# Performance work log

Hardware: AMD Instinct MI355X
Metric: run time of the kernel (lower is better)

The kernel has to match this reference:

```python
import jax, jax.numpy as jnp
import numpy as np

H = 512        # num_hidden
Z = 512        # latent_len
TIME = 0.2
N_STEPS = 4    # fixed-step RK4 replaces adaptive dopri5 (same dynamics math)
B, N = 4, 4096


def _linear_params(k, fin, fout):
    k1, k2 = jax.random.split(k)
    s = 1.0 / np.sqrt(fin)
    W = jax.random.uniform(k1, (fout, fin), minval=-s, maxval=s, dtype=jnp.float32)
    b = jax.random.uniform(k2, (fout,), minval=-s, maxval=s, dtype=jnp.float32)
    return W, b


def setup_inputs() -> dict:
    key = jax.random.key(0)
    ks = jax.random.split(key, 16)
    inp = {
        "code": jax.random.normal(ks[0], (B, 1, Z), dtype=jnp.float32),
        "x": jax.random.uniform(ks[1], (B, N, 3), dtype=jnp.float32),
    }
    dims = {"l1": (3, H), "l2": (H, H), "l3": (H, H), "l4": (H, 3), "cond": (Z, H)}
    i = 2
    for f in ("f1", "f2"):
        for name, (fin, fout) in dims.items():
            W, b = _linear_params(ks[i], fin, fout)
            i += 1
            inp[f + "_" + name + "_w"] = W
            inp[f + "_" + name + "_b"] = b
    return inp


def _node_block(x, sf, W1, b1, W2, b2, W3, b3, W4, b4):
    """Fixed-step RK4 integration of ODEFunc dynamics over [0, TIME].
    x: (B,N,3) point state; sf: (B,1,H) precomputed tanh(cond(code)) shape features
    (constant along the trajectory since the latent code has zero dynamics)."""
    def dyn(p):
        pf = jax.nn.relu(p @ W1.T + b1)          # (B,N,H) point features
        h = pf * sf                               # gated point-shape features
        h = jax.nn.relu(h @ W2.T + b2) + h        # residual stage 1
        h = jax.nn.relu(h @ W3.T + b3) + h        # residual stage 2
        return jnp.tanh(h @ W4.T + b4)            # (B,N,3) flow direction

    dt = TIME / N_STEPS
    def step(p, _):
        k1 = dyn(p)
        k2 = dyn(p + 0.5 * dt * k1)
        k3 = dyn(p + 0.5 * dt * k2)
        k4 = dyn(p + dt * k3)
        return p + (dt / 6.0) * (k1 + 2.0 * k2 + 2.0 * k3 + k4), None

    x, _ = jax.lax.scan(step, x, None, length=N_STEPS)
    return x


def reference(code, x,
              f1_l1_w, f1_l1_b, f1_l2_w, f1_l2_b, f1_l3_w, f1_l3_b,
              f1_l4_w, f1_l4_b, f1_cond_w, f1_cond_b,
              f2_l1_w, f2_l1_b, f2_l2_w, f2_l2_b, f2_l3_w, f2_l3_b,
              f2_l4_w, f2_l4_b, f2_cond_w, f2_cond_b):
    sf1 = jnp.tanh(code @ f1_cond_w.T + f1_cond_b)  # (B,1,H), broadcasts over N
    x = _node_block(x, sf1, f1_l1_w, f1_l1_b, f1_l2_w, f1_l2_b,
                    f1_l3_w, f1_l3_b, f1_l4_w, f1_l4_b)
    sf2 = jnp.tanh(code @ f2_cond_w.T + f2_cond_b)
    x = _node_block(x, sf2, f2_l1_w, f2_l1_b, f2_l2_w, f2_l2_b,
                    f2_l3_w, f2_l3_b, f2_l4_w, f2_l4_b)
    return x  # pred_y: (B,N,3)
```

## Files before the change

### kernel.cpp

```cpp
#include <hip/hip_runtime.h>
#include <stdint.h>

typedef short short8 __attribute__((ext_vector_type(8)));
typedef float floatx16 __attribute__((ext_vector_type(16)));

#define NPTS 16384
#define TILE_M 64
#define THREADS 1024
#define PA 2
#define PB 4

__device__ inline unsigned short f2bf(float f) {
  __bf16 h = (__bf16)f;
  return __builtin_bit_cast(unsigned short, h);
}
__device__ inline float bf2f(unsigned short h) {
  union { unsigned u; float f; } v; v.u = ((unsigned)h) << 16;
  return v.f;
}

__global__
__attribute__((amdgpu_flat_work_group_size(THREADS, THREADS),
               amdgpu_waves_per_eu(4, 4)))
void node_kernel(
    const float* __restrict__ x, float* __restrict__ outp,
    const unsigned short* __restrict__ wbf, const float* __restrict__ sfall,
    const float* __restrict__ w1a, const float* __restrict__ b1a,
    const float* __restrict__ b2a, const float* __restrict__ b3a,
    const float* __restrict__ w4a, const float* __restrict__ b4a,
    const float* __restrict__ w1b, const float* __restrict__ b1b,
    const float* __restrict__ b2b, const float* __restrict__ b3b,
    const float* __restrict__ w4b, const float* __restrict__ b4b)
{
  __shared__ unsigned short act[TILE_M][520];
  __shared__ float pcur4[TILE_M][4];
  __shared__ float pev4[TILE_M][4];
  __shared__ float kac4[TILE_M][4];
  __shared__ float w4s[3][512];

  const int tid = threadIdx.x;
  const int wg = blockIdx.x;
  const int m0 = wg * TILE_M;
  const int batch = wg >> 6;
  const int lane = tid & 63;
  const int wid = tid >> 6;

  if (tid < TILE_M * 3) {
    int m = tid / 3, c = tid % 3;
    float v = x[m0 * 3 + tid];
    pcur4[m][c] = v;
    pev4[m][c] = v;
  }
  __syncthreads();

  const int aBase = (lane & 31) * 1040 + (lane >> 5) * 16;
  const char* actB = (const char*)&act[0][0];
  const int bcol = wid * 64 + lane;

  const int p1col = tid & 511;
  const int p1r0 = (tid >> 9) * 32;

  const float dt = 0.05f;

  #pragma unroll 1
  for (int f = 0; f < 2; ++f) {
    const float* w1 = f ? w1b : w1a;
    const float* b1v = f ? b1b : b1a;
    const float* b2v = f ? b2b : b2a;
    const float* b3v = f ? b3b : b3a;
    const float* w4 = f ? w4b : w4a;
    const float* b4v = f ? b4b : b4a;
    const short8* w2p = (const short8*)(wbf + (size_t)(f * 2 + 0) * 262144) + bcol;
    const short8* w3p = (const short8*)(wbf + (size_t)(f * 2 + 1) * 262144) + bcol;

    const float ww0 = w1[p1col * 3 + 0], ww1 = w1[p1col * 3 + 1], ww2 = w1[p1col * 3 + 2];
    const float bb = b1v[p1col];
    const float ss = sfall[f * 2048 + batch * 512 + p1col];
    const float b40 = b4v[0], b41 = b4v[1], b42 = b4v[2];

    for (int i = tid; i < 1536; i += THREADS) ((float*)w4s)[i] = w4[i];
    __syncthreads();

    #pragma unroll 1
    for (int st = 0; st < 4; ++st) {
      #pragma unroll 1
      for (int stage = 0; stage < 4; ++stage) {
        short8 bq[PB];
        #pragma unroll
        for (int i = 0; i < PB - 1; ++i) bq[i] = w2p[i * 1024];

        #pragma unroll 4
        for (int mi = 0; mi < 32; ++mi) {
          int m = p1r0 + mi;
          const float4 pv = *(const float4*)&pev4[m][0];
          float v = fmaf(pv.x, ww0, fmaf(pv.y, ww1, fmaf(pv.z, ww2, bb)));
          v = fmaxf(v, 0.f) * ss;
          act[m][p1col] = f2bf(v);
        }
        __syncthreads();

        #pragma unroll 1
        for (int s = 0; s < 2; ++s) {
          const float* bias = s ? b3v : b2v;
          const short8* bp = s ? w3p : w2p;
          floatx16 acc0{}, acc1{};
          short8 aq0[PA], aq1[PA];
          #pragma unroll
          for (int i = 0; i < PA - 1; ++i) {
            aq0[i] = *(const short8*)(actB + aBase + i * 32);
            aq1[i] = *(const short8*)(actB + aBase + 33280 + i * 32);
          }

          #pragma unroll
          for (int kt = 0; kt < 32; ++kt) {
            int la = kt + PA - 1;
            if (la < 32) {
              aq0[la % PA] = *(const short8*)(actB + aBase + la * 32);
              aq1[la % PA] = *(const short8*)(actB + aBase + 33280 + la * 32);
            }
            int lb = kt + PB - 1;
            if (lb < 32) bq[lb % PB] = bp[lb * 1024];
            acc0 = __builtin_amdgcn_mfma_f32_32x32x16_bf16(aq0[kt % PA], bq[kt % PB], acc0, 0, 0, 0);
            acc1 = __builtin_amdgcn_mfma_f32_32x32x16_bf16(aq1[kt % PA], bq[kt % PB], acc1, 0, 0, 0);
          }

          if (s == 0) {
            #pragma unroll
            for (int i = 0; i < PB - 1; ++i) bq[i] = w3p[i * 1024];
          }

          __syncthreads();
          {
            int ncol = wid * 32 + (lane & 31);
            float bs = bias[ncol];
            int rbase = 4 * (lane >> 5);
            #pragma unroll
            for (int g = 0; g < 4; ++g) {
              float r0[4], r1[4];
              #pragma unroll
              for (int i = 0; i < 4; ++i) {
                int row = i + 8 * g + rbase;
                r0[i] = bf2f(act[row][ncol]);
                r1[i] = bf2f(act[32 + row][ncol]);
              }
              #pragma unroll
              for (int i = 0; i < 4; ++i) {
                int row = i + 8 * g + rbase;
                float v = fmaxf(acc0[g * 4 + i] + bs, 0.f) + r0[i];
                act[row][ncol] = f2bf(v);
                v = fmaxf(acc1[g * 4 + i] + bs, 0.f) + r1[i];
                act[32 + row][ncol] = f2bf(v);
              }
            }
          }
          __syncthreads();
        }

        {
          int m = tid >> 4, jj = tid & 15;
          const unsigned short* arow = &act[m][0];
          float s0 = 0.f, s1 = 0.f, s2 = 0.f;
          #pragma unroll
          for (int c = 0; c < 4; ++c) {
            int k0 = (c * 16 + jj) * 8;
            short8 av = *(const short8*)(arow + k0);
            #pragma unroll
            for (int half = 0; half < 2; ++half) {
              float4 wv0 = *(const float4*)&w4s[0][k0 + half * 4];
              float4 wv1 = *(const float4*)&w4s[1][k0 + half * 4];
              float4 wv2 = *(const float4*)&w4s[2][k0 + half * 4];
              #pragma unroll
              for (int e = 0; e < 4; ++e) {
                float a = bf2f((unsigned short)av[half * 4 + e]);
                s0 = fmaf(a, ((const float*)&wv0)[e], s0);
                s1 = fmaf(a, ((const float*)&wv1)[e], s1);
                s2 = fmaf(a, ((const float*)&wv2)[e], s2);
              }
            }
          }
          s0 += __shfl_xor(s0, 1); s1 += __shfl_xor(s1, 1); s2 += __shfl_xor(s2, 1);
          s0 += __shfl_xor(s0, 2); s1 += __shfl_xor(s1, 2); s2 += __shfl_xor(s2, 2);
          s0 += __shfl_xor(s0, 4); s1 += __shfl_xor(s1, 4); s2 += __shfl_xor(s2, 4);
          s0 += __shfl_xor(s0, 8); s1 += __shfl_xor(s1, 8); s2 += __shfl_xor(s2, 8);
          if (jj < 3) {
            float sv = (jj == 0) ? s0 : ((jj == 1) ? s1 : s2);
            float bv = (jj == 0) ? b40 : ((jj == 1) ? b41 : b42);
            float fl = tanhf(sv + bv);
            float pc = pcur4[m][jj];
            if (stage == 0) {
              kac4[m][jj] = fl;
              pev4[m][jj] = fmaf(0.5f * dt, fl, pc);
            } else if (stage == 1) {
              kac4[m][jj] += 2.f * fl;
              pev4[m][jj] = fmaf(0.5f * dt, fl, pc);
            } else if (stage == 2) {
              kac4[m][jj] += 2.f * fl;
              pev4[m][jj] = fmaf(dt, fl, pc);
            } else {
              float np = fmaf(dt / 6.f, kac4[m][jj] + fl, pc);
              pcur4[m][jj] = np;
              pev4[m][jj] = np;
            }
          }
        }
        __syncthreads();
      }
    }
  }

  if (tid < TILE_M * 3) outp[m0 * 3 + tid] = pcur4[tid / 3][tid % 3];
}

__global__ void setup_shuffle(const float* s0, const float* s1, const float* s2,
                              const float* s3, unsigned short* dst) {
  int idx = blockIdx.x * blockDim.x + threadIdx.x;
  int w = idx >> 15;
  int r = idx & 32767;
  int lane = r & 63;
  int tile = r >> 6;
  int nt = tile & 15, kt = tile >> 4;
  const float* W = (w == 0) ? s0 : (w == 1) ? s1 : (w == 2) ? s2 : s3;
  int n = nt * 32 + (lane & 31);
  int k0 = kt * 16 + (lane >> 5) * 8;
  const float* src = W + n * 512 + k0;
  unsigned short* d = dst + ((size_t)w << 18) + (size_t)r * 8;
  #pragma unroll
  for (int j = 0; j < 8; ++j) d[j] = f2bf(src[j]);
}

__global__ void setup_sf(const float* code, const float* cw1, const float* cb1,
                         const float* cw2, const float* cb2, float* sfout) {
  int f = blockIdx.x >> 2, b = blockIdx.x & 3;
  const float* cw = f ? cw2 : cw1;
  const float* cb = f ? cb2 : cb1;
  int j = threadIdx.x;
  const float* c = code + b * 512;
  float s = cb[j];
  for (int k = 0; k < 512; ++k) s = fmaf(c[k], cw[j * 512 + k], s);
  sfout[f * 2048 + b * 512 + j] = tanhf(s);
}

extern "C" void kernel_launch(void* const* d_in, const int* in_sizes, int n_in,
                              void* d_out, int out_size, void* d_ws, size_t ws_size,
                              hipStream_t stream) {
  const float* code = (const float*)d_in[0];
  const float* x    = (const float*)d_in[1];
  char* ws = (char*)d_ws;
  float* sf = (float*)ws;
  unsigned short* wbf = (unsigned short*)(ws + 16384);

  setup_shuffle<<<512, 256, 0, stream>>>((const float*)d_in[4], (const float*)d_in[6],
                                         (const float*)d_in[14], (const float*)d_in[16], wbf);
  setup_sf<<<8, 512, 0, stream>>>(code, (const float*)d_in[10], (const float*)d_in[11],
                                  (const float*)d_in[20], (const float*)d_in[21], sf);

  node_kernel<<<NPTS / TILE_M, THREADS, 0, stream>>>(x, (float*)d_out, wbf, sf,
      (const float*)d_in[2], (const float*)d_in[3], (const float*)d_in[5],
      (const float*)d_in[7], (const float*)d_in[8], (const float*)d_in[9],
      (const float*)d_in[12], (const float*)d_in[13], (const float*)d_in[15],
      (const float*)d_in[17], (const float*)d_in[18], (const float*)d_in[19]);
}
```

Baseline: 835.7 us.

## Split MFMA tiles by row-half so each wave reuses A across two column tiles

Each wave previously computed two 32-row tiles against one 32-column weight tile, loading two A fragments and one B fragment per k-step. Now each wave owns one 32-row half and two column tiles, loading one A fragment from LDS and two B fragments from global per k-step. This cuts LDS reads for A but doubles the per-wave global weight fragment loads and the registers held for B prefetch. It also rearranges the W4 copy in shared memory into a padded per-chunk layout, which may change bank conflicts in the final projection.

```diff
diff --git a/kernel.cpp b/kernel.cpp
--- a/kernel.cpp
+++ b/kernel.cpp
@@ -36,7 +36,7 @@
   __shared__ float pcur4[TILE_M][4];
   __shared__ float pev4[TILE_M][4];
   __shared__ float kac4[TILE_M][4];
-  __shared__ float w4s[3][512];
+  __shared__ float w4c[64][28];
 
   const int tid = threadIdx.x;
   const int wg = blockIdx.x;
@@ -44,6 +44,8 @@
   const int batch = wg >> 6;
   const int lane = tid & 63;
   const int wid = tid >> 6;
+  const int rowhalf = wid & 1;
+  const int cp = wid >> 1;
 
   if (tid < TILE_M * 3) {
     int m = tid / 3, c = tid % 3;
@@ -53,9 +55,10 @@
   }
   __syncthreads();
 
-  const int aBase = (lane & 31) * 1040 + (lane >> 5) * 16;
+  const int aBase = (lane & 31) * 1040 + (lane >> 5) * 16 + rowhalf * 33280;
   const char* actB = (const char*)&act[0][0];
-  const int bcol = wid * 64 + lane;
+  const int bcol0 = cp * 128 + lane;
+  const int bcol1 = bcol0 + 64;
 
   const int p1col = tid & 511;
   const int p1r0 = (tid >> 9) * 32;
@@ -70,24 +73,32 @@
     const float* b3v = f ? b3b : b3a;
     const float* w4 = f ? w4b : w4a;
     const float* b4v = f ? b4b : b4a;
-    const short8* w2p = (const short8*)(wbf + (size_t)(f * 2 + 0) * 262144) + bcol;
-    const short8* w3p = (const short8*)(wbf + (size_t)(f * 2 + 1) * 262144) + bcol;
+    const short8* w2p0 = (const short8*)(wbf + (size_t)(f * 2 + 0) * 262144) + bcol0;
+    const short8* w2p1 = (const short8*)(wbf + (size_t)(f * 2 + 0) * 262144) + bcol1;
+    const short8* w3p0 = (const short8*)(wbf + (size_t)(f * 2 + 1) * 262144) + bcol0;
+    const short8* w3p1 = (const short8*)(wbf + (size_t)(f * 2 + 1) * 262144) + bcol1;
 
     const float ww0 = w1[p1col * 3 + 0], ww1 = w1[p1col * 3 + 1], ww2 = w1[p1col * 3 + 2];
     const float bb = b1v[p1col];
     const float ss = sfall[f * 2048 + batch * 512 + p1col];
     const float b40 = b4v[0], b41 = b4v[1], b42 = b4v[2];
 
-    for (int i = tid; i < 1536; i += THREADS) ((float*)w4s)[i] = w4[i];
+    for (int i = tid; i < 64 * 24; i += THREADS) {
+      int q = i / 24, r = i % 24;
+      w4c[q][r] = w4[(r >> 3) * 512 + q * 8 + (r & 7)];
+    }
     __syncthreads();
 
     #pragma unroll 1
     for (int st = 0; st < 4; ++st) {
       #pragma unroll 1
       for (int stage = 0; stage < 4; ++stage) {
-        short8 bq[PB];
+        short8 bq0[PB], bq1[PB];
         #pragma unroll
-        for (int i = 0; i < PB - 1; ++i) bq[i] = w2p[i * 1024];
+        for (int i = 0; i < PB - 1; ++i) {
+          bq0[i] = w2p0[i * 1024];
+          bq1[i] = w2p1[i * 1024];
+        }
 
         #pragma unroll 4
         for (int mi = 0; mi < 32; ++mi) {
@@ -102,54 +113,58 @@
         #pragma unroll 1
         for (int s = 0; s < 2; ++s) {
           const float* bias = s ? b3v : b2v;
-          const short8* bp = s ? w3p : w2p;
+          const short8* bp0 = s ? w3p0 : w2p0;
+          const short8* bp1 = s ? w3p1 : w2p1;
           floatx16 acc0{}, acc1{};
-          short8 aq0[PA], aq1[PA];
+          short8 aq[PA];
           #pragma unroll
-          for (int i = 0; i < PA - 1; ++i) {
-            aq0[i] = *(const short8*)(actB + aBase + i * 32);
-            aq1[i] = *(const short8*)(actB + aBase + 33280 + i * 32);
-          }
+          for (int i = 0; i < PA - 1; ++i)
+            aq[i] = *(const short8*)(actB + aBase + i * 32);
 
           #pragma unroll
           for (int kt = 0; kt < 32; ++kt) {
             int la = kt + PA - 1;
-            if (la < 32) {
-              aq0[la % PA] = *(const short8*)(actB + aBase + la * 32);
-              aq1[la % PA] = *(const short8*)(actB + aBase + 33280 + la * 32);
-            }
+            if (la < 32)
+              aq[la % PA] = *(const short8*)(actB + aBase + la * 32);
             int lb = kt + PB - 1;
-            if (lb < 32) bq[lb % PB] = bp[lb * 1024];
-            acc0 = __builtin_amdgcn_mfma_f32_32x32x16_bf16(aq0[kt % PA], bq[kt % PB], acc0, 0, 0, 0);
-            acc1 = __builtin_amdgcn_mfma_f32_32x32x16_bf16(aq1[kt % PA], bq[kt % PB], acc1, 0, 0, 0);
+            if (lb < 32) {
+              bq0[lb % PB] = bp0[lb * 1024];
+              bq1[lb % PB] = bp1[lb * 1024];
+            }
+            acc0 = __builtin_amdgcn_mfma_f32_32x32x16_bf16(aq[kt % PA], bq0[kt % PB], acc0, 0, 0, 0);
+            acc1 = __builtin_amdgcn_mfma_f32_32x32x16_bf16(aq[kt % PA], bq1[kt % PB], acc1, 0, 0, 0);
           }
 
           if (s == 0) {
             #pragma unroll
-            for (int i = 0; i < PB - 1; ++i) bq[i] = w3p[i * 1024];
+            for (int i = 0; i < PB - 1; ++i) {
+              bq0[i] = w3p0[i * 1024];
+              bq1[i] = w3p1[i * 1024];
+            }
           }
 
           __syncthreads();
           {
-            int ncol = wid * 32 + (lane & 31);
-            float bs = bias[ncol];
-            int rbase = 4 * (lane >> 5);
+            int ncol0 = cp * 64 + (lane & 31);
+            int ncol1 = ncol0 + 32;
+            float bs0 = bias[ncol0], bs1 = bias[ncol1];
+            int rbase = rowhalf * 32 + 4 * (lane >> 5);
             #pragma unroll
             for (int g = 0; g < 4; ++g) {
               float r0[4], r1[4];
               #pragma unroll
               for (int i = 0; i < 4; ++i) {
                 int row = i + 8 * g + rbase;
-                r0[i] = bf2f(act[row][ncol]);
-                r1[i] = bf2f(act[32 + row][ncol]);
+                r0[i] = bf2f(act[row][ncol0]);
+                r1[i] = bf2f(act[row][ncol1]);
               }
               #pragma unroll
               for (int i = 0; i < 4; ++i) {
                 int row = i + 8 * g + rbase;
-                float v = fmaxf(acc0[g * 4 + i] + bs, 0.f) + r0[i];
-                act[row][ncol] = f2bf(v);
-                v = fmaxf(acc1[g * 4 + i] + bs, 0.f) + r1[i];
-                act[32 + row][ncol] = f2bf(v);
+                float v = fmaxf(acc0[g * 4 + i] + bs0, 0.f) + r0[i];
+                act[row][ncol0] = f2bf(v);
+                v = fmaxf(acc1[g * 4 + i] + bs1, 0.f) + r1[i];
+                act[row][ncol1] = f2bf(v);
               }
             }
           }
@@ -162,13 +177,15 @@
           float s0 = 0.f, s1 = 0.f, s2 = 0.f;
           #pragma unroll
           for (int c = 0; c < 4; ++c) {
-            int k0 = (c * 16 + jj) * 8;
+            int q = c * 16 + jj;
+            int k0 = q * 8;
             short8 av = *(const short8*)(arow + k0);
+            const float* wc = &w4c[q][0];
             #pragma unroll
             for (int half = 0; half < 2; ++half) {
-              float4 wv0 = *(const float4*)&w4s[0][k0 + half * 4];
-              float4 wv1 = *(const float4*)&w4s[1][k0 + half * 4];
-              float4 wv2 = *(const float4*)&w4s[2][k0 + half * 4];
+              float4 wv0 = *(const float4*)(wc + 0 + half * 4);
+              float4 wv1 = *(const float4*)(wc + 8 + half * 4);
+              float4 wv2 = *(const float4*)(wc + 16 + half * 4);
               #pragma unroll
               for (int e = 0; e < 4; ++e) {
                 float a = bf2f((unsigned short)av[half * 4 + e]);
```

After: 945.1 us. 1.13x slower.
